# Kernel optimization log

Measured on AMD Instinct MI355X. Metric: run time of the kernel, lower is better.

## Reference

```python
import jax, jax.numpy as jnp
import numpy as np

RADIUS = 2
TEMP = 1.0
B, CIN, D, H, W = 1, 32, 64, 64, 64
PROJ, OUT = 64, 64
K = (2 * RADIUS + 1) ** 3  # 125 local offsets

_OFFSETS = np.array([(dz, dy, dx)
                     for dz in range(-RADIUS, RADIUS + 1)
                     for dy in range(-RADIUS, RADIUS + 1)
                     for dx in range(-RADIUS, RADIUS + 1)], dtype=np.int32)


def _conv3d(x, w, b, pad):
    y = jax.lax.conv_general_dilated(
        x, w, window_strides=(1, 1, 1), padding=[(pad, pad)] * 3,
        dimension_numbers=('NCDHW', 'OIDHW', 'NCDHW'))
    if b is not None:
        y = y + b[None, :, None, None, None]
    return y


def _l2norm(x):
    # torch F.normalize(dim=1): x / max(||x||_2, 1e-12)
    n = jnp.sqrt(jnp.sum(x * x, axis=1, keepdims=True))
    return x / jnp.maximum(n, 1e-12)


def _inorm(x, eps=1e-5):
    # InstanceNorm3d (affine=False): normalize over spatial dims per (B,C)
    mu = jnp.mean(x, axis=(2, 3, 4), keepdims=True)
    var = jnp.mean((x - mu) ** 2, axis=(2, 3, 4), keepdims=True)
    return (x - mu) * jax.lax.rsqrt(var + eps)


def _ntn(x):
    return jnp.nan_to_num(x, nan=0.0, posinf=0.0, neginf=0.0)


def setup_inputs() -> dict:
    key = jax.random.key(0)
    ks = jax.random.split(key, 8)
    s = 0.05
    return {
        'source_features': jax.random.normal(ks[0], (B, CIN, D, H, W), jnp.float32),
        'warped_target_features': jax.random.normal(ks[1], (B, CIN, D, H, W), jnp.float32),
        'w_src': jax.random.normal(ks[2], (PROJ, CIN, 1, 1, 1), jnp.float32) * s,
        'b_src': jnp.zeros((PROJ,), jnp.float32),
        'w_tgt': jax.random.normal(ks[3], (PROJ, CIN, 1, 1, 1), jnp.float32) * s,
        'b_tgt': jnp.zeros((PROJ,), jnp.float32),
        'w_enc1': jax.random.normal(ks[4], (OUT, K + 5, 3, 3, 3), jnp.float32) * s,
        'b_enc1': jnp.zeros((OUT,), jnp.float32),
        'w_enc2': jax.random.normal(ks[5], (OUT, OUT, 3, 3, 3), jnp.float32) * s,
        'b_enc2': jnp.zeros((OUT,), jnp.float32),
    }


def reference(source_features, warped_target_features, w_src, b_src, w_tgt, b_tgt,
              w_enc1, b_enc1, w_enc2, b_enc2):
    sp = _l2norm(_conv3d(source_features, w_src, b_src, 0))      # [B,P,D,H,W]
    tp = _l2norm(_conv3d(warped_target_features, w_tgt, b_tgt, 0))
    pt = jnp.pad(tp, ((0, 0), (0, 0), (RADIUS, RADIUS), (RADIUS, RADIUS), (RADIUS, RADIUS)),
                 mode='edge')  # replicate pad

    starts = jnp.asarray(_OFFSETS + RADIUS, jnp.int32)  # [K,3] slice starts

    def corr_one(st):
        sh = jax.lax.dynamic_slice(pt, (0, 0, st[0], st[1], st[2]), (B, PROJ, D, H, W))
        return jnp.sum(sp * sh, axis=1)  # [B,D,H,W]

    corr = jnp.transpose(jax.vmap(corr_one)(starts), (1, 0, 2, 3, 4))  # [B,K,D,H,W]
    scaled = corr / max(TEMP, 1e-6)

    top2 = jax.lax.top_k(jnp.moveaxis(scaled, 1, -1), 2)[0]  # [B,D,H,W,2]
    m = jnp.moveaxis(top2[..., 0:1], -1, 1)   # running max   [B,1,D,H,W]
    s2 = jnp.moveaxis(top2[..., 1:2], -1, 1)  # second max

    p = jnp.exp(scaled - m)                    # [B,K,D,H,W]
    Z = jnp.sum(p, axis=1, keepdims=True)
    inv = 1.0 / jnp.maximum(Z, 1e-8)

    offv = jnp.asarray(_OFFSETS, jnp.float32)  # [K,3]
    expected_offset = _ntn(jnp.einsum('bkdhw,kc->bcdhw', p, offv) * inv)
    confidence = _ntn(jnp.minimum(inv, 1.0))   # max-prob = exp(m-m)/Z
    second_prob = jnp.exp(s2 - m) * inv
    margin = _ntn(jnp.maximum(confidence - second_prob, 0.0))
    entropy = _ntn(m + jnp.log(jnp.maximum(Z, 1e-8))
                   - jnp.sum(p * scaled, axis=1, keepdims=True) * inv)

    enc_in = jnp.concatenate([corr, expected_offset, confidence, entropy], axis=1)  # [B,K+5,D,H,W]
    h = _conv3d(enc_in, w_enc1, b_enc1, 1)
    h = jax.nn.gelu(_inorm(h), approximate=False)
    h = _conv3d(h, w_enc2, b_enc2, 1)
    h = jax.nn.gelu(_inorm(h), approximate=False)
    encoded_features = _ntn(h)

    return expected_offset, confidence, margin, entropy, encoded_features
```

## Files before the change

kernel.cpp:

```cpp
#include <hip/hip_runtime.h>

#define DEV __device__ __forceinline__

typedef short bf16x8 __attribute__((ext_vector_type(8)));
typedef float f32x4 __attribute__((ext_vector_type(4)));

static const int NVOX = 262144;

DEV float bflo(unsigned int u) { return __uint_as_float(u << 16); }
DEV float bfhi(unsigned int u) { return __uint_as_float(u & 0xffff0000u); }
DEV float bf2f(unsigned short s) { return __uint_as_float(((unsigned int)s) << 16); }
DEV unsigned short f2bf(float f) {
    unsigned int x = __float_as_uint(f);
    x += 0x7fffu + ((x >> 16) & 1u);
    return (unsigned short)(x >> 16);
}
DEV float ldin(const void* p, int i, int f) {
    return f ? ((const float*)p)[i] : bf2f(((const unsigned short*)p)[i]);
}

__global__ void sniff_kernel(const unsigned short* __restrict__ src, int* __restrict__ flag) {
    __shared__ int cnt[256];
    int t = threadIdx.x;
    int c = 0;
    for (int i = t; i < 4096; i += 256) {
        unsigned int u = (unsigned int)src[i] & 0x7fffu;
        c += (u >= 0x4900u) ? 1 : 0;
    }
    cnt[t] = c;
    __syncthreads();
    for (int s = 128; s > 0; s >>= 1) {
        if (t < s) cnt[t] += cnt[t + s];
        __syncthreads();
    }
    if (t == 0) *flag = (cnt[0] > 8) ? 1 : 0;
}

__global__ void prep_kernel(const void* __restrict__ w1, const void* __restrict__ w2,
                            const void* __restrict__ bsv, const void* __restrict__ btv,
                            const void* __restrict__ b1v, const void* __restrict__ b2v,
                            const int* __restrict__ flag,
                            unsigned short* __restrict__ Wf1,
                            unsigned short* __restrict__ Wf2,
                            float* __restrict__ fbias) {
    const int f = *flag;
    int idx = blockIdx.x * 256 + threadIdx.x;
    const int N1  = 27 * 4 * 4 * 512;
    const int N1E = 2 * 4 * 512;
    const int N2  = 27 * 2 * 4 * 512;
    if (idx < N1) {
        int frag = idx >> 9;
        int r    = idx & 511;
        int lane = r >> 3, j = r & 7;
        int nt = frag & 3;
        int tk = frag >> 2;
        int tap = tk >> 2, kc = tk & 3;
        int o  = nt * 16 + (lane & 15);
        int cp = kc * 32 + (lane >> 4) * 8 + j;
        Wf1[idx] = f2bf(ldin(w1, (o * 130 + cp) * 27 + tap, f));
    } else if (idx < N1 + N1E) {
        int i2 = idx - N1;
        int frag = i2 >> 9;
        int r    = i2 & 511;
        int lane = r >> 3, j = r & 7;
        int nt = frag & 3, kc = frag >> 2;
        int o   = nt * 16 + (lane & 15);
        int kap = kc * 32 + (lane >> 4) * 8 + j;
        unsigned short val = 0;
        if (kap < 54) {
            int tap = kap >> 1, ch = 128 + (kap & 1);
            val = f2bf(ldin(w1, (o * 130 + ch) * 27 + tap, f));
        }
        Wf1[idx] = val;
    } else if (idx < N1 + N1E + N2) {
        int i2 = idx - N1 - N1E;
        int frag = i2 >> 9;
        int r    = i2 & 511;
        int lane = r >> 3, j = r & 7;
        int nt = frag & 3;
        int tk = frag >> 2;
        int tap = tk >> 1, kc = tk & 1;
        int o = nt * 16 + (lane & 15);
        int c = kc * 32 + (lane >> 4) * 8 + j;
        Wf2[i2] = f2bf(ldin(w2, (o * 64 + c) * 27 + tap, f));
    } else if (idx < N1 + N1E + N2 + 256) {
        int j = idx - N1 - N1E - N2;
        const void* bp = (j < 64) ? bsv : (j < 128) ? btv : (j < 192) ? b1v : b2v;
        fbias[j] = ldin(bp, j & 63, f);
    }
}

__global__ __launch_bounds__(256) void proj_kernel(
        const void* __restrict__ Xsrc, const void* __restrict__ Xtgt,
        const void* __restrict__ Wsrc, const void* __restrict__ Wtgt,
        const float* __restrict__ fbias, const int* __restrict__ flag,
        unsigned short* __restrict__ SP, unsigned short* __restrict__ TP) {
    const int f = *flag;
    const void* Xin = blockIdx.y ? Xtgt : Xsrc;
    const void* W   = blockIdx.y ? Wtgt : Wsrc;
    const float* Bb = fbias + (blockIdx.y ? 64 : 0);
    unsigned short* Outp = blockIdx.y ? TP : SP;

    __shared__ float ws[2048];
    const int t = threadIdx.x;
    for (int i = t; i < 2048; i += 256) {
        int ci = i >> 6, o = i & 63;
        ws[i] = ldin(W, o * 32 + ci, f);
    }
    __syncthreads();

    const size_t v = (size_t)blockIdx.x * 256 + t;
    float acc[64];
#pragma unroll
    for (int o = 0; o < 64; ++o) acc[o] = Bb[o];
    if (f) {
        const float* Xf = (const float*)Xin;
        for (int ci = 0; ci < 32; ++ci) {
            float x = Xf[(size_t)ci * NVOX + v];
            const float4* wr = (const float4*)(ws + ci * 64);
#pragma unroll
            for (int o4 = 0; o4 < 16; ++o4) {
                float4 w4 = wr[o4];
                acc[o4 * 4 + 0] = fmaf(w4.x, x, acc[o4 * 4 + 0]);
                acc[o4 * 4 + 1] = fmaf(w4.y, x, acc[o4 * 4 + 1]);
                acc[o4 * 4 + 2] = fmaf(w4.z, x, acc[o4 * 4 + 2]);
                acc[o4 * 4 + 3] = fmaf(w4.w, x, acc[o4 * 4 + 3]);
            }
        }
    } else {
        const unsigned short* Xb = (const unsigned short*)Xin;
        for (int ci = 0; ci < 32; ++ci) {
            float x = bf2f(Xb[(size_t)ci * NVOX + v]);
            const float4* wr = (const float4*)(ws + ci * 64);
#pragma unroll
            for (int o4 = 0; o4 < 16; ++o4) {
                float4 w4 = wr[o4];
                acc[o4 * 4 + 0] = fmaf(w4.x, x, acc[o4 * 4 + 0]);
                acc[o4 * 4 + 1] = fmaf(w4.y, x, acc[o4 * 4 + 1]);
                acc[o4 * 4 + 2] = fmaf(w4.z, x, acc[o4 * 4 + 2]);
                acc[o4 * 4 + 3] = fmaf(w4.w, x, acc[o4 * 4 + 3]);
            }
        }
    }
    float s = 0.f;
#pragma unroll
    for (int o = 0; o < 64; ++o) s = fmaf(acc[o], acc[o], s);
    float scale = 1.f / fmaxf(sqrtf(s), 1e-12f);

    unsigned int pk[32];
#pragma unroll
    for (int o = 0; o < 32; ++o)
        pk[o] = (unsigned int)f2bf(acc[2 * o] * scale) |
                ((unsigned int)f2bf(acc[2 * o + 1] * scale) << 16);
    uint4* outp = (uint4*)(Outp + v * 64);
#pragma unroll
    for (int j = 0; j < 8; ++j)
        outp[j] = make_uint4(pk[4 * j], pk[4 * j + 1], pk[4 * j + 2], pk[4 * j + 3]);
}

DEV void tp_load(const unsigned short* __restrict__ TP, int t, int z, int y,
                 int it, uint4* pre) {
    const int zc = min(max(z + it / 5 - 2, 0), 63);
    const int yc = min(max(y + it % 5 - 2, 0), 63);
    const unsigned short* tbase = TP + ((size_t)zc * 64 + yc) * 4096;
#pragma unroll
    for (int j = 0; j < 3; ++j) {
        int i = t + j * 256;
        uint4 vv = make_uint4(0u, 0u, 0u, 0u);
        if (i < 640) {
            int pp = i >> 3, cc = i & 7;
            int xc = min(max(pp - 2, 0), 63);
            vv = *(const uint4*)(tbase + xc * 64 + cc * 8);
        }
        pre[j] = vv;
    }
}

DEV void tp_commit(unsigned short* buf, int t, const uint4* pre) {
#pragma unroll
    for (int j = 0; j < 3; ++j) {
        int i = t + j * 256;
        if (i < 640) {
            int pp = i >> 3, cc = i & 7;
            *(uint4*)((char*)buf + pp * 128 + ((cc ^ (pp & 7)) * 16)) = pre[j];
        }
    }
}

__global__ __launch_bounds__(256) void corr_kernel(
        const unsigned short* __restrict__ SP, const unsigned short* __restrict__ TP,
        unsigned short* __restrict__ X1, float* __restrict__ Out) {
    __shared__ __align__(16) unsigned short spb[64 * 64];
    __shared__ __align__(16) unsigned short tpb[2][80 * 64];
    __shared__ __align__(16) unsigned short stage[64 * 168];
    __shared__ __align__(16) float band[64 * 5];

    const int t = threadIdx.x;
    const int wv = t >> 6, lane = t & 63;
    const int q = lane >> 4, l16 = lane & 15;
    const int x0 = wv * 16;

    const int bid = blockIdx.x;
    const int wg = (bid & 7) * 512 + (bid >> 3);
    const int z = wg >> 6, y = wg & 63;
    const size_t vbase = ((size_t)z * 64 + y) * 64;

    uint4 spv0, spv1;
    {
        int i0 = t, i1 = t + 256;
        spv0 = *(const uint4*)(SP + (vbase + (i0 >> 3)) * 64 + (i0 & 7) * 8);
        spv1 = *(const uint4*)(SP + (vbase + (i1 >> 3)) * 64 + (i1 & 7) * 8);
    }
    {
        int vox = t >> 2, c4 = t & 3;
        *(uint4*)(&stage[vox * 168 + 128 + c4 * 8]) = make_uint4(0u, 0u, 0u, 0u);
    }
    {
        int i0 = t, i1 = t + 256;
        int xa = i0 >> 3, ca = i0 & 7;
        int xb = i1 >> 3, cb = i1 & 7;
        *(uint4*)((char*)spb + xa * 128 + ((ca ^ (xa & 7)) * 16)) = spv0;
        *(uint4*)((char*)spb + xb * 128 + ((cb ^ (xb & 7)) * 16)) = spv1;
    }

    float m = -1e30f, s2 = -1e30f, Zs = 0.f, S1 = 0.f, Ox = 0.f, Oy = 0.f, Oz = 0.f;

    uint4 pre[3];
    tp_load(TP, t, z, y, 0, pre);
    int p = 0;
    for (int it = 0; it < 25; ++it) {
        tp_commit(tpb[p], t, pre);
        __syncthreads();
        if (it < 24) tp_load(TP, t, z, y, it + 1, pre);

        f32x4 acc[2] = {{0.f, 0.f, 0.f, 0.f}, {0.f, 0.f, 0.f, 0.f}};
        {
            const char* sb = (const char*)spb;
            const char* tb = (const char*)tpb[p];
            const int xr = x0 + l16;
#pragma unroll
            for (int kc = 0; kc < 2; ++kc) {
                bf16x8 a = *(const bf16x8*)(sb + xr * 128 + (((kc * 4 + q) ^ (xr & 7)) * 16));
#pragma unroll
                for (int nt = 0; nt < 2; ++nt) {
                    const int pr = x0 + nt * 16 + l16;
                    bf16x8 b = *(const bf16x8*)(tb + pr * 128 + (((kc * 4 + q) ^ (pr & 7)) * 16));
                    acc[nt] = __builtin_amdgcn_mfma_f32_16x16x32_bf16(a, b, acc[nt], 0, 0, 0);
                }
            }
        }
        const int kb = it * 5;
#pragma unroll
        for (int nt = 0; nt < 2; ++nt) {
#pragma unroll
            for (int r = 0; r < 4; ++r) {
                int ml = q * 4 + r;
                int dxp = nt * 16 + l16 - ml;
                if ((unsigned)dxp < 5u) {
                    int xl = x0 + ml;
                    float d = acc[nt][r];
                    band[xl * 5 + dxp] = d;
                    stage[xl * 168 + kb + dxp] = f2bf(d);
                }
            }
        }
        __syncthreads();
        if (t < 64) {
            const float fz = (float)(it / 5 - 2), fy = (float)(it % 5 - 2);
#pragma unroll
            for (int dxp = 0; dxp < 5; ++dxp) {
                float d = band[t * 5 + dxp];
                float fx = (float)(dxp - 2);
                if (d > m) {
                    float sc = __expf(m - d);
                    Zs = fmaf(Zs, sc, 1.f); S1 = fmaf(S1, sc, d);
                    Ox = fmaf(Ox, sc, fx); Oy = fmaf(Oy, sc, fy); Oz = fmaf(Oz, sc, fz);
                    s2 = m; m = d;
                } else {
                    float e = __expf(d - m);
                    Zs += e; S1 = fmaf(e, d, S1);
                    Ox = fmaf(e, fx, Ox); Oy = fmaf(e, fy, Oy); Oz = fmaf(e, fz, Oz);
                    s2 = fmaxf(s2, d);
                }
            }
        }
        p ^= 1;
    }

    if (t < 64) {
        float inv  = 1.f / fmaxf(Zs, 1e-8f);
        float eoz = Oz * inv, eoy = Oy * inv, eox = Ox * inv;
        float conf = fminf(inv, 1.f);
        float marg = fmaxf(conf - __expf(s2 - m) * inv, 0.f);
        float ent  = m + __logf(fmaxf(Zs, 1e-8f)) - S1 * inv;
        stage[t * 168 + 125] = f2bf(eoz);
        stage[t * 168 + 126] = f2bf(eoy);
        stage[t * 168 + 127] = f2bf(eox);
        stage[t * 168 + 128] = f2bf(conf);
        stage[t * 168 + 129] = f2bf(ent);
        const size_t v = vbase + t;
        Out[v]                    = eoz;
        Out[(size_t)NVOX + v]     = eoy;
        Out[(size_t)2 * NVOX + v] = eox;
        Out[(size_t)3 * NVOX + v] = conf;
        Out[(size_t)4 * NVOX + v] = marg;
        Out[(size_t)5 * NVOX + v] = ent;
    }
    __syncthreads();

#pragma unroll
    for (int j = 0; j < 5; ++j) {
        int i = t + j * 256;
        int vox = i / 20, cc = i % 20;
        *(uint4*)(X1 + (vbase + vox) * 160 + (size_t)cc * 8) =
            *(const uint4*)(&stage[vox * 168 + cc * 8]);
    }
}

template <int XSTRIDE, int CPAD, int LSTRIDE, int KC, int NLD, bool TAIL>
__global__ __launch_bounds__(256) void conv3_kernel(
        const unsigned short* __restrict__ Xin, const unsigned short* __restrict__ Wf,
        const unsigned short* __restrict__ Wfe,
        const float* __restrict__ Bias, unsigned short* __restrict__ Out) {
    __shared__ unsigned short rowbuf[2][66 * LSTRIDE];
    const int lin = blockIdx.x;
    const int z = (lin & 7) * 8 + ((lin >> 3) >> 6);
    const int y = (lin >> 3) & 63;
    const int t = threadIdx.x;
    const int wv = t >> 6, lane = t & 63;
    const int quad = lane >> 4, l16 = lane & 15;
    const int mt2 = (wv & 1) * 2;
    const int nt2 = (wv >> 1) * 2;
    const int CH16 = CPAD / 8;

    f32x4 acc[2][2] = {{{0.f,0.f,0.f,0.f},{0.f,0.f,0.f,0.f}},
                       {{0.f,0.f,0.f,0.f},{0.f,0.f,0.f,0.f}}};

    uint4 pre[NLD];
    {
        const int zz = z - 1, yy = y - 1;
        const bool valid = (unsigned)zz < 64u && (unsigned)yy < 64u;
        const unsigned short* base = Xin + (((size_t)(valid ? zz : 0) * 64 + (valid ? yy : 0)) * 64) * XSTRIDE;
#pragma unroll
        for (int i = 0; i < NLD; ++i) {
            int idx = t + i * 256;
            uint4 val = make_uint4(0u, 0u, 0u, 0u);
            if (idx < 66 * CH16) {
                int xi = idx / CH16, ci = idx % CH16;
                int gx = xi - 1;
                if (valid && gx >= 0 && gx < 64) val = *(const uint4*)(base + gx * XSTRIDE + ci * 8);
            }
            pre[i] = val;
        }
    }

    if (TAIL) {
        unsigned short* ebuf = &rowbuf[1][0];
#pragma unroll
        for (int i2 = 0; i2 < 8; ++i2) {
            int i = t + i2 * 256;
            int vox = i >> 5, slot = i & 31;
            unsigned int val = 0u;
            int kap;
            if (slot < 27) {
                int dz = slot / 9 - 1, dy = (slot / 3) % 3 - 1, dxx = slot % 3 - 1;
                int zz = z + dz, yy = y + dy, xx = vox + dxx;
                kap = slot * 2;
                if ((unsigned)zz < 64u && (unsigned)yy < 64u && (unsigned)xx < 64u)
                    val = *(const unsigned int*)(Xin + (((size_t)zz * 64 + yy) * 64 + xx) * XSTRIDE + 128);
            } else {
                kap = 54 + (slot - 27) * 2;
            }
            *(unsigned int*)(ebuf + vox * 72 + kap) = val;
        }
        __syncthreads();
#pragma unroll
        for (int kc = 0; kc < 2; ++kc) {
            bf16x8 bte[2];
#pragma unroll
            for (int nl = 0; nl < 2; ++nl)
                bte[nl] = *(const bf16x8*)(Wfe + (size_t)(kc * 4 + nt2 + nl) * 512 + lane * 8);
#pragma unroll
            for (int ml = 0; ml < 2; ++ml) {
                bf16x8 a = *(const bf16x8*)(ebuf + ((mt2 + ml) * 16 + l16) * 72 + (kc * 4 + quad) * 8);
#pragma unroll
                for (int nl = 0; nl < 2; ++nl)
                    acc[ml][nl] = __builtin_amdgcn_mfma_f32_16x16x32_bf16(a, bte[nl], acc[ml][nl], 0, 0, 0);
            }
        }
        __syncthreads();
    }

    int p = 0;
    for (int it = 0; it < 9; ++it) {
#pragma unroll
        for (int i = 0; i < NLD; ++i) {
            int idx = t + i * 256;
            if (idx < 66 * CH16) {
                int xi = idx / CH16, ci = idx % CH16;
                *(uint4*)(&rowbuf[p][xi * LSTRIDE + ci * 8]) = pre[i];
            }
        }
        __syncthreads();
        if (it < 8) {
            const int itn = it + 1;
            const int zz = z + itn / 3 - 1, yy = y + itn % 3 - 1;
            const bool valid = (unsigned)zz < 64u && (unsigned)yy < 64u;
            const unsigned short* base = Xin + (((size_t)(valid ? zz : 0) * 64 + (valid ? yy : 0)) * 64) * XSTRIDE;
#pragma unroll
            for (int i = 0; i < NLD; ++i) {
                int idx = t + i * 256;
                uint4 val = make_uint4(0u, 0u, 0u, 0u);
                if (idx < 66 * CH16) {
                    int xi = idx / CH16, ci = idx % CH16;
                    int gx = xi - 1;
                    if (valid && gx >= 0 && gx < 64) val = *(const uint4*)(base + gx * XSTRIDE + ci * 8);
                }
                pre[i] = val;
            }
        }
        const unsigned short* rp = rowbuf[p];
#pragma unroll
        for (int dx = 0; dx < 3; ++dx) {
            const int tap = it * 3 + dx;
            const unsigned short* wt = Wf + ((size_t)tap * KC * 4) * 512 + lane * 8;
            bf16x8 bf[KC][2];
#pragma unroll
            for (int kc = 0; kc < KC; ++kc)
#pragma unroll
                for (int nl = 0; nl < 2; ++nl)
                    bf[kc][nl] = *(const bf16x8*)(wt + (size_t)(kc * 4 + nt2 + nl) * 512);
#pragma unroll
            for (int kc = 0; kc < KC; ++kc) {
#pragma unroll
                for (int ml = 0; ml < 2; ++ml) {
                    bf16x8 a = *(const bf16x8*)(&rp[((mt2 + ml) * 16 + l16 + dx) * LSTRIDE + kc * 32 + quad * 8]);
#pragma unroll
                    for (int nl = 0; nl < 2; ++nl)
                        acc[ml][nl] = __builtin_amdgcn_mfma_f32_16x16x32_bf16(a, bf[kc][nl], acc[ml][nl], 0, 0, 0);
                }
            }
        }
        p ^= 1;
    }

    const size_t vbase = ((size_t)z * 64 + y) * 64;
#pragma unroll
    for (int ml = 0; ml < 2; ++ml) {
#pragma unroll
        for (int nl = 0; nl < 2; ++nl) {
            const int oc = (nt2 + nl) * 16 + l16;
            const float bv = Bias[oc];
#pragma unroll
            for (int r = 0; r < 4; ++r)
                Out[(vbase + (mt2 + ml) * 16 + quad * 4 + r) * 64 + oc] = f2bf(acc[ml][nl][r] + bv);
        }
    }
}

__global__ __launch_bounds__(256) void stats_kernel(
        const unsigned short* __restrict__ H, float* __restrict__ stats) {
    const int t = threadIdx.x;
    const int c = t & 63, g = t >> 6;
    float s = 0.f, q = 0.f;
    for (int v = blockIdx.x * 4 + g; v < NVOX; v += gridDim.x * 4) {
        float x = bf2f(H[(size_t)v * 64 + c]);
        s += x; q = fmaf(x, x, q);
    }
    __shared__ float ls[256], lq[256];
    ls[t] = s; lq[t] = q;
    __syncthreads();
    if (t < 64) {
        s = ls[t] + ls[t + 64] + ls[t + 128] + ls[t + 192];
        q = lq[t] + lq[t + 64] + lq[t + 128] + lq[t + 192];
        atomicAdd(&stats[c], s);
        atomicAdd(&stats[64 + c], q);
    }
}

__global__ void finalize_kernel(const float* __restrict__ stats, float* __restrict__ musr) {
    int c = threadIdx.x;
    if (c < 64) {
        float mu  = stats[c] * (1.0f / 262144.0f);
        float var = stats[64 + c] * (1.0f / 262144.0f) - mu * mu;
        musr[c] = mu;
        musr[64 + c] = rsqrtf(var + 1e-5f);
    }
}

__global__ __launch_bounds__(256) void norm_gelu_kernel(
        const unsigned short* __restrict__ H, const float* __restrict__ musr,
        unsigned short* __restrict__ G) {
    const size_t base = ((size_t)blockIdx.x * 256 + threadIdx.x) * 8;
    uint4 u = *(const uint4*)(H + base);
    const int c0 = (int)(base & 63);
    const unsigned int uu[4] = {u.x, u.y, u.z, u.w};
    unsigned int w[4];
#pragma unroll
    for (int p = 0; p < 4; ++p) {
        int c = c0 + p * 2;
        float x0 = (bflo(uu[p]) - musr[c]) * musr[64 + c];
        float x1 = (bfhi(uu[p]) - musr[c + 1]) * musr[64 + c + 1];
        float g0 = 0.5f * x0 * (1.f + erff(x0 * 0.70710678118f));
        float g1 = 0.5f * x1 * (1.f + erff(x1 * 0.70710678118f));
        w[p] = (unsigned int)f2bf(g0) | ((unsigned int)f2bf(g1) << 16);
    }
    *(uint4*)(G + base) = make_uint4(w[0], w[1], w[2], w[3]);
}

__global__ __launch_bounds__(256) void out_final_kernel(
        const unsigned short* __restrict__ H2, const float* __restrict__ musr,
        float* __restrict__ OutEnc) {
    __shared__ float tile[64 * 260];
    const int t = threadIdx.x;
    const size_t v0 = (size_t)blockIdx.x * 256;
#pragma unroll
    for (int i = 0; i < 8; ++i) {
        int chunk = t + i * 256;
        uint4 u = *(const uint4*)(H2 + v0 * 64 + (size_t)chunk * 8);
        int vox = chunk >> 3;
        int c0 = (chunk & 7) * 8;
        const unsigned int uu[4] = {u.x, u.y, u.z, u.w};
#pragma unroll
        for (int p = 0; p < 4; ++p) {
            int c = c0 + p * 2;
            float x0 = (bflo(uu[p]) - musr[c]) * musr[64 + c];
            float x1 = (bfhi(uu[p]) - musr[c + 1]) * musr[64 + c + 1];
            tile[c * 260 + vox]       = 0.5f * x0 * (1.f + erff(x0 * 0.70710678118f));
            tile[(c + 1) * 260 + vox] = 0.5f * x1 * (1.f + erff(x1 * 0.70710678118f));
        }
    }
    __syncthreads();
    const int c = t >> 2, sub = t & 3;
#pragma unroll
    for (int iter = 0; iter < 16; ++iter) {
        int fq = iter * 4 + sub;
        float4 val = *(const float4*)(&tile[c * 260 + fq * 4]);
        *(float4*)(OutEnc + (size_t)c * NVOX + v0 + fq * 4) = val;
    }
}

extern "C" void kernel_launch(void* const* d_in, const int* in_sizes, int n_in,
                              void* d_out, int out_size, void* d_ws, size_t ws_size,
                              hipStream_t stream) {
    const void* src  = d_in[0];
    const void* tgt  = d_in[1];
    const void* wsrc = d_in[2];
    const void* bsrc = d_in[3];
    const void* wtgt = d_in[4];
    const void* btgt = d_in[5];
    const void* w1   = d_in[6];
    const void* b1   = d_in[7];
    const void* w2   = d_in[8];
    const void* b2   = d_in[9];
    float* out = (float*)d_out;

    char* ws = (char*)d_ws;
    unsigned short* TPb = (unsigned short*)(ws);
    unsigned short* SPb = (unsigned short*)(ws + 33554432);
    unsigned short* X1  = (unsigned short*)(ws + 67108864);
    unsigned short* Wf1 = (unsigned short*)(ws + 150994944);
    unsigned short* Wf2 = (unsigned short*)(ws + 151547904);
    int*   flag   = (int*)  (ws + 151769088);
    float* fbias  = (float*)(ws + 151769152);
    float* stats1 = (float*)(ws + 151770176);
    float* musr1  = (float*)(ws + 151770688);
    float* stats2 = (float*)(ws + 151771200);
    float* musr2  = (float*)(ws + 151771712);
    unsigned short* H1 = SPb;
    unsigned short* G1 = TPb;
    unsigned short* H2 = X1;
    unsigned short* Wf1e = Wf1 + 27 * 4 * 4 * 512;

    (void)hipMemsetAsync(stats1, 0, 2048, stream);
    sniff_kernel<<<1, 256, 0, stream>>>((const unsigned short*)src, flag);
    prep_kernel<<<1313, 256, 0, stream>>>(w1, w2, bsrc, btgt, b1, b2, flag, Wf1, Wf2, fbias);
    proj_kernel<<<dim3(1024, 2), 256, 0, stream>>>(src, tgt, wsrc, wtgt, fbias, flag, SPb, TPb);
    corr_kernel<<<4096, 256, 0, stream>>>(SPb, TPb, X1, out);
    conv3_kernel<160, 128, 136, 4, 5, true><<<4096, 256, 0, stream>>>(X1, Wf1, Wf1e, fbias + 128, H1);
    stats_kernel<<<256, 256, 0, stream>>>(H1, stats1);
    finalize_kernel<<<1, 64, 0, stream>>>(stats1, musr1);
    norm_gelu_kernel<<<8192, 256, 0, stream>>>(H1, musr1, G1);
    conv3_kernel<64, 64, 72, 2, 3, false><<<4096, 256, 0, stream>>>(G1, Wf2, nullptr, fbias + 192, H2);
    stats_kernel<<<256, 256, 0, stream>>>(H2, stats2);
    finalize_kernel<<<1, 64, 0, stream>>>(stats2, musr2);
    out_final_kernel<<<1024, 256, 0, stream>>>(H2, musr2, out + 6 * (size_t)NVOX);
}
```

Before: 794.3 us.

## Move corr softmax stats out of the loop into a parallel 4-thread reduction

Drops the per-iteration serial online-softmax, which ran on only 64 threads behind an extra barrier on each of the 25 iterations. The bf16 correlation band is now written to an XOR-swizzled LDS stage. After the loop, four threads per voxel compute max, second max, Z, entropy and expected offset, then combine their partial results with shuffles. Statistics now come from bf16-rounded correlations, and X1 padding channels 130-159 are no longer explicitly zeroed. That is only safe if the downstream conv ignores them or the buffer is already cleared.

```diff
diff --git a/kernel.cpp b/kernel.cpp
--- a/kernel.cpp
+++ b/kernel.cpp
@@ -192,8 +192,7 @@
         unsigned short* __restrict__ X1, float* __restrict__ Out) {
     __shared__ __align__(16) unsigned short spb[64 * 64];
     __shared__ __align__(16) unsigned short tpb[2][80 * 64];
-    __shared__ __align__(16) unsigned short stage[64 * 168];
-    __shared__ __align__(16) float band[64 * 5];
+    __shared__ __align__(16) unsigned short stage[64 * 128];
 
     const int t = threadIdx.x;
     const int wv = t >> 6, lane = t & 63;
@@ -205,25 +204,15 @@
     const int z = wg >> 6, y = wg & 63;
     const size_t vbase = ((size_t)z * 64 + y) * 64;
 
-    uint4 spv0, spv1;
     {
         int i0 = t, i1 = t + 256;
-        spv0 = *(const uint4*)(SP + (vbase + (i0 >> 3)) * 64 + (i0 & 7) * 8);
-        spv1 = *(const uint4*)(SP + (vbase + (i1 >> 3)) * 64 + (i1 & 7) * 8);
-    }
-    {
-        int vox = t >> 2, c4 = t & 3;
-        *(uint4*)(&stage[vox * 168 + 128 + c4 * 8]) = make_uint4(0u, 0u, 0u, 0u);
-    }
-    {
-        int i0 = t, i1 = t + 256;
+        uint4 spv0 = *(const uint4*)(SP + (vbase + (i0 >> 3)) * 64 + (i0 & 7) * 8);
+        uint4 spv1 = *(const uint4*)(SP + (vbase + (i1 >> 3)) * 64 + (i1 & 7) * 8);
         int xa = i0 >> 3, ca = i0 & 7;
         int xb = i1 >> 3, cb = i1 & 7;
         *(uint4*)((char*)spb + xa * 128 + ((ca ^ (xa & 7)) * 16)) = spv0;
         *(uint4*)((char*)spb + xb * 128 + ((cb ^ (xb & 7)) * 16)) = spv1;
     }
-
-    float m = -1e30f, s2 = -1e30f, Zs = 0.f, S1 = 0.f, Ox = 0.f, Oy = 0.f, Oz = 0.f;
 
     uint4 pre[3];
     tp_load(TP, t, z, y, 0, pre);
@@ -250,6 +239,7 @@
             }
         }
         const int kb = it * 5;
+        char* sg = (char*)stage;
 #pragma unroll
         for (int nt = 0; nt < 2; ++nt) {
 #pragma unroll
@@ -258,62 +248,102 @@
                 int dxp = nt * 16 + l16 - ml;
                 if ((unsigned)dxp < 5u) {
                     int xl = x0 + ml;
-                    float d = acc[nt][r];
-                    band[xl * 5 + dxp] = d;
-                    stage[xl * 168 + kb + dxp] = f2bf(d);
+                    *(unsigned short*)(sg + xl * 256 + (((kb + dxp) * 2) ^ ((xl & 7) << 4))) =
+                        f2bf(acc[nt][r]);
                 }
             }
         }
-        __syncthreads();
-        if (t < 64) {
-            const float fz = (float)(it / 5 - 2), fy = (float)(it % 5 - 2);
-#pragma unroll
-            for (int dxp = 0; dxp < 5; ++dxp) {
-                float d = band[t * 5 + dxp];
-                float fx = (float)(dxp - 2);
-                if (d > m) {
-                    float sc = __expf(m - d);
-                    Zs = fmaf(Zs, sc, 1.f); S1 = fmaf(S1, sc, d);
-                    Ox = fmaf(Ox, sc, fx); Oy = fmaf(Oy, sc, fy); Oz = fmaf(Oz, sc, fz);
-                    s2 = m; m = d;
-                } else {
-                    float e = __expf(d - m);
-                    Zs += e; S1 = fmaf(e, d, S1);
-                    Ox = fmaf(e, fx, Ox); Oy = fmaf(e, fy, Oy); Oz = fmaf(e, fz, Oz);
-                    s2 = fmaxf(s2, d);
-                }
-            }
-        }
         p ^= 1;
     }
 
-    if (t < 64) {
-        float inv  = 1.f / fmaxf(Zs, 1e-8f);
-        float eoz = Oz * inv, eoy = Oy * inv, eox = Ox * inv;
-        float conf = fminf(inv, 1.f);
-        float marg = fmaxf(conf - __expf(s2 - m) * inv, 0.f);
-        float ent  = m + __logf(fmaxf(Zs, 1e-8f)) - S1 * inv;
-        stage[t * 168 + 125] = f2bf(eoz);
-        stage[t * 168 + 126] = f2bf(eoy);
-        stage[t * 168 + 127] = f2bf(eox);
-        stage[t * 168 + 128] = f2bf(conf);
-        stage[t * 168 + 129] = f2bf(ent);
-        const size_t v = vbase + t;
-        Out[v]                    = eoz;
-        Out[(size_t)NVOX + v]     = eoy;
-        Out[(size_t)2 * NVOX + v] = eox;
-        Out[(size_t)3 * NVOX + v] = conf;
-        Out[(size_t)4 * NVOX + v] = marg;
-        Out[(size_t)5 * NVOX + v] = ent;
-    }
     __syncthreads();
-
-#pragma unroll
-    for (int j = 0; j < 5; ++j) {
+    {
+        const int vox = t >> 2, part = t & 3;
+        const int sx = (vox & 7) << 4;
+        const char* sg = (const char*)stage;
+        uint4 u[4];
+#pragma unroll
+        for (int j = 0; j < 4; ++j)
+            u[j] = *(const uint4*)(sg + vox * 256 + ((part * 64 + j * 16) ^ sx));
+
+        float m = -1e30f, s2 = -1e30f;
+#pragma unroll
+        for (int j = 0; j < 4; ++j) {
+            const unsigned int uu[4] = {u[j].x, u[j].y, u[j].z, u[j].w};
+#pragma unroll
+            for (int w = 0; w < 4; ++w) {
+                int k = part * 32 + j * 8 + w * 2;
+                float d0 = (k < 125) ? bflo(uu[w]) : -1e30f;
+                float d1 = (k + 1 < 125) ? bfhi(uu[w]) : -1e30f;
+                float lo0 = fminf(d0, m); m = fmaxf(d0, m); s2 = fmaxf(s2, lo0);
+                float lo1 = fminf(d1, m); m = fmaxf(d1, m); s2 = fmaxf(s2, lo1);
+            }
+        }
+#pragma unroll
+        for (int off = 1; off <= 2; off <<= 1) {
+            float om = __shfl_xor(m, off, 64);
+            float os = __shfl_xor(s2, off, 64);
+            float lo = fminf(m, om);
+            m = fmaxf(m, om);
+            s2 = fmaxf(fmaxf(s2, os), lo);
+        }
+        int kk = part * 32;
+        int dz0 = kk / 25, rem = kk - dz0 * 25, dy0 = rem / 5, dx0 = rem - dy0 * 5;
+        float fx = (float)(dx0 - 2), fy = (float)(dy0 - 2), fz = (float)(dz0 - 2);
+        float Zs = 0.f, S1 = 0.f, Ox = 0.f, Oy = 0.f, Oz = 0.f;
+#pragma unroll
+        for (int j = 0; j < 4; ++j) {
+            const unsigned int uu[4] = {u[j].x, u[j].y, u[j].z, u[j].w};
+#pragma unroll
+            for (int w = 0; w < 8; ++w) {
+                int k = part * 32 + j * 8 + w;
+                bool ok = (k < 125);
+                float d = (w & 1) ? bfhi(uu[w >> 1]) : bflo(uu[w >> 1]);
+                d = ok ? d : 0.f;
+                float e = ok ? __expf(d - m) : 0.f;
+                Zs += e; S1 = fmaf(e, d, S1);
+                Ox = fmaf(e, fx, Ox); Oy = fmaf(e, fy, Oy); Oz = fmaf(e, fz, Oz);
+                fx += 1.f;
+                if (fx > 2.5f) { fx = -2.f; fy += 1.f; if (fy > 2.5f) { fy = -2.f; fz += 1.f; } }
+            }
+        }
+#pragma unroll
+        for (int off = 1; off <= 2; off <<= 1) {
+            Zs += __shfl_xor(Zs, off, 64);
+            S1 += __shfl_xor(S1, off, 64);
+            Ox += __shfl_xor(Ox, off, 64);
+            Oy += __shfl_xor(Oy, off, 64);
+            Oz += __shfl_xor(Oz, off, 64);
+        }
+        if (part == 0) {
+            float inv  = 1.f / fmaxf(Zs, 1e-8f);
+            float eoz = Oz * inv, eoy = Oy * inv, eox = Ox * inv;
+            float conf = fminf(inv, 1.f);
+            float marg = fmaxf(conf - __expf(s2 - m) * inv, 0.f);
+            float ent  = m + __logf(fmaxf(Zs, 1e-8f)) - S1 * inv;
+            char* sgw = (char*)stage;
+            *(unsigned short*)(sgw + vox * 256 + (250 ^ sx)) = f2bf(eoz);
+            *(unsigned short*)(sgw + vox * 256 + (252 ^ sx)) = f2bf(eoy);
+            *(unsigned short*)(sgw + vox * 256 + (254 ^ sx)) = f2bf(eox);
+            const size_t v = vbase + vox;
+            *(unsigned int*)(X1 + v * 160 + 128) =
+                (unsigned int)f2bf(conf) | ((unsigned int)f2bf(ent) << 16);
+            Out[v]                    = eoz;
+            Out[(size_t)NVOX + v]     = eoy;
+            Out[(size_t)2 * NVOX + v] = eox;
+            Out[(size_t)3 * NVOX + v] = conf;
+            Out[(size_t)4 * NVOX + v] = marg;
+            Out[(size_t)5 * NVOX + v] = ent;
+        }
+    }
+    __syncthreads();
+
+#pragma unroll
+    for (int j = 0; j < 4; ++j) {
         int i = t + j * 256;
-        int vox = i / 20, cc = i % 20;
+        int vox = i >> 4, cc = i & 15;
         *(uint4*)(X1 + (vbase + vox) * 160 + (size_t)cc * 8) =
-            *(const uint4*)(&stage[vox * 168 + cc * 8]);
+            *(const uint4*)((const char*)stage + vox * 256 + ((cc * 16) ^ ((vox & 7) << 4)));
     }
 }
 
```

Result: faster. 736.0 us (-7.3%).
